# Optimization experiments

Measured on AMD Instinct MI355X. Metric: run time of the kernel, lower is better.

## Reference

```python
import jax, jax.numpy as jnp
import numpy as np
from jax import lax

EPS = 1e-31
V, L, B, T = 30000, 400, 16, 145
E, EH, DH, ENC, COMB = 100, 150, 200, 300, 500
SOS = 1


def setup_inputs() -> dict:
    key = jax.random.key(0)
    ks = jax.random.split(key, 32)
    def p(i, shape):
        return jax.random.normal(ks[i], shape, dtype=jnp.float32) * 0.05
    return {
        "input_tensor": jax.random.randint(ks[0], (L, B), 0, V),
        "embedding": p(1, (V, E)),
        "enc_Wih_f": p(2, (3 * EH, E)), "enc_Whh_f": p(3, (3 * EH, EH)),
        "enc_bih_f": p(4, (3 * EH,)), "enc_bhh_f": p(5, (3 * EH,)),
        "enc_Wih_b": p(6, (3 * EH, E)), "enc_Whh_b": p(7, (3 * EH, EH)),
        "enc_bih_b": p(8, (3 * EH,)), "enc_bhh_b": p(9, (3 * EH,)),
        "adapter_W": p(10, (DH, ENC)), "adapter_b": p(11, (DH,)),
        "dec_Wih": p(12, (3 * DH, E)), "dec_Whh": p(13, (3 * DH, DH)),
        "dec_bih": p(14, (3 * DH,)), "dec_bhh": p(15, (3 * DH,)),
        "bil_W": p(16, (1, DH, ENC)), "bil_b": p(17, (1,)),
        "cover_weight": jax.random.uniform(ks[18], (1,), dtype=jnp.float32),
        "ptr_W": p(19, (1, COMB)), "ptr_b": p(20, (1,)),
        "preout_W": p(21, (E, COMB)), "preout_b": p(22, (E,)),
        "out_b": p(23, (V,)),
    }


def _gru_cell(x, h, Wih, Whh, bih, bhh):
    # torch GRU cell semantics (gates ordered r, z, n)
    gi = x @ Wih.T + bih
    gh = h @ Whh.T + bhh
    ir, iz, i_n = jnp.split(gi, 3, axis=-1)
    hr, hz, hn = jnp.split(gh, 3, axis=-1)
    r = jax.nn.sigmoid(ir + hr)
    z = jax.nn.sigmoid(iz + hz)
    n = jnp.tanh(i_n + r * hn)
    return (1.0 - z) * n + z * h


def _run_gru(emb, Wih, Whh, bih, bhh):
    # emb: [L, B, E] -> outputs [L, B, H], final hidden [B, H]
    h0 = jnp.zeros((emb.shape[1], Whh.shape[1]), emb.dtype)
    def step(h, x):
        h = _gru_cell(x, h, Wih, Whh, bih, bhh)
        return h, h
    hT, ys = lax.scan(step, h0, emb)
    return ys, hT


def reference(input_tensor, embedding,
              enc_Wih_f, enc_Whh_f, enc_bih_f, enc_bhh_f,
              enc_Wih_b, enc_Whh_b, enc_bih_b, enc_bhh_b,
              adapter_W, adapter_b,
              dec_Wih, dec_Whh, dec_bih, dec_bhh,
              bil_W, bil_b, cover_weight,
              ptr_W, ptr_b, preout_W, preout_b, out_b):
    # ----- encoder: bidirectional single-layer GRU -----
    emb = embedding[input_tensor]                       # [L, B, E]
    out_f, h_f = _run_gru(emb, enc_Wih_f, enc_Whh_f, enc_bih_f, enc_bhh_f)
    out_r, h_b = _run_gru(emb[::-1], enc_Wih_b, enc_Whh_b, enc_bih_b, enc_bhh_b)
    enc_out = jnp.concatenate([out_f, out_r[::-1]], axis=-1)   # [L, B, 300]
    enc_hidden = jnp.concatenate([h_f, h_b], axis=-1)          # [B, 300]
    h0 = enc_hidden @ adapter_W.T + adapter_b                  # enc_dec_adapter -> [B, 200]

    enc_word_idx = input_tensor.T                              # [B, L]
    batch_idx = jnp.arange(enc_out.shape[1])[:, None]

    # ----- decoder: greedy loop with enc attention + coverage + pointer-gen -----
    def dec_step(carry, _):
        h, cover, tok = carry
        x = embedding[tok]                                     # [B, E]
        h = _gru_cell(x, h, dec_Wih, dec_Whh, dec_bih, dec_bhh)
        # bilinear energy: h W e + b, plus coverage term
        hW = h @ bil_W[0]                                      # [B, 300]
        energy = jnp.einsum('be,lbe->lb', hW, enc_out) + bil_b[0]
        energy = energy + cover_weight[0] * jnp.log(cover.T + EPS)
        attn = jax.nn.softmax(energy, axis=0)                  # [L, B], softmax over enc steps
        context = jnp.einsum('lbe,lb->be', enc_out, attn)      # [B, 300]
        combined = jnp.concatenate([h, context], axis=-1)      # [B, 500]
        pre = combined @ preout_W.T + preout_b                 # [B, 100]
        logits = pre @ embedding.T + out_b                     # tied output embedding [B, V]
        p_ptr = jax.nn.sigmoid(combined @ ptr_W.T + ptr_b)     # [B, 1]
        gen = jax.nn.softmax(logits, axis=1)
        attn_bl = attn.T                                       # [B, L]
        out = (1.0 - p_ptr) * gen
        out = out.at[batch_idx, enc_word_idx].add(p_ptr * attn_bl)
        new_tok = jnp.argmax(out, axis=1)
        return (h, cover + attn_bl, new_tok), out

    cover0 = jnp.zeros(enc_word_idx.shape, emb.dtype)
    tok0 = jnp.full((enc_out.shape[1],), SOS, dtype=input_tensor.dtype)
    _, outputs = lax.scan(dec_step, (h0, cover0, tok0), None, length=T)
    return outputs  # [T, B, V] pointer-generator mixture probabilities
```

## Files before the change

kernel.cpp:

```cpp
#include <hip/hip_runtime.h>

namespace {

constexpr int Vv=30000, Ll=400, Bb=16, Tt=145;
constexpr int Ee=100, EHh=150, DHh=200, ENc=300;
constexpr int SOS_TOK=1;
constexpr int NB=256, NT=512;

constexpr long SO_EMB = 0;
constexpr long SO_GIF = SO_EMB + 6400L*100;
constexpr long SO_GIB = SO_GIF + 6400L*450;
constexpr long SO_ENC = SO_GIB + 6400L*450;
constexpr long SO_WCAT= SO_GIF;

constexpr int RH    = 0;
constexpr int REXP  = 3200;
constexpr int RCTX  = 9600;
constexpr int RPREH = 22912;
constexpr int RPSUM = 24576;
constexpr int RPMAX = 28672;
constexpr int RCAND = 36864;
constexpr int RING_SZ = 49664;

constexpr long OFF_M    = 0;
constexpr long OFF_N    = OFF_M + 6400L*200;
constexpr long OFF_Q    = OFF_N + 6400L*100;
constexpr long OFF_HENC = OFF_Q + 6400;
constexpr long OFF_H0   = OFF_HENC + 4800;
constexpr long OFF_COVER= OFF_H0 + 3200;
constexpr long OFF_R143 = OFF_COVER + 8192;
constexpr long OFF_R144 = OFF_R143 + RING_SZ;
constexpr long WS_F32_END = OFF_R144 + RING_SZ;
constexpr long IWS_BYTE  = ((WS_F32_END*4 + 255)/256)*256;
constexpr int ISVL=0, IGV=6400, IGLS=12800, ICG0=19216, INGR=23328;
constexpr long BAR_BYTE  = ((IWS_BYTE + 23344L*4 + 255)/256)*256;
constexpr int FH  =0;
constexpr int FS1 =256;
constexpr int FCTX=320;
constexpr int FS4 =448;
constexpr int ABRT=704;

struct Args {
  const int* itok;
  const float* emb;
  const float* Wfih; const float* Wfhh; const float* bfih; const float* bfhh;
  const float* Wbih; const float* Wbhh; const float* bbih; const float* bbhh;
  const float* adW; const float* adb;
  const float* dWih; const float* dWhh; const float* dbih; const float* dbhh;
  const float* bilW; const float* bilb; const float* cw;
  const float* ptrW; const float* ptrb;
  const float* preW; const float* preb; const float* outb;
  float* out; float* ws; int* iws; int* bar;
};

__device__ __forceinline__ int chunkStart(int c){ return c*117 + (c<48? c:48); }
__device__ __forceinline__ int chunkSize(int c){ return 117 + (c<48?1:0); }
__device__ __forceinline__ float sigm(float x){ return 1.f/(1.f+expf(-x)); }
__device__ __forceinline__ unsigned long long packvi(float val, int v){
  return ((unsigned long long)__float_as_uint(val)<<32) | (unsigned)(~(unsigned)v);
}
__device__ __forceinline__ void ast(float* p, float v){
  __hip_atomic_store(p, v, __ATOMIC_RELAXED, __HIP_MEMORY_SCOPE_AGENT); }
__device__ __forceinline__ void astu(unsigned long long* p, unsigned long long v){
  __hip_atomic_store(p, v, __ATOMIC_RELAXED, __HIP_MEMORY_SCOPE_AGENT); }
__device__ __forceinline__ int aldi(const int* p){
  return __hip_atomic_load(p, __ATOMIC_RELAXED, __HIP_MEMORY_SCOPE_AGENT); }
__device__ __forceinline__ void asti(int* p, int v){
  __hip_atomic_store(p, v, __ATOMIC_RELAXED, __HIP_MEMORY_SCOPE_AGENT); }

__device__ __forceinline__ float* ringBase(const Args& a, int t){
  if (t<=142) return a.out + (long)(t+2)*480000;
  return a.ws + (t==143 ? OFF_R143 : OFF_R144);
}

__device__ __forceinline__ void setFlag(int* f, int v){
  asm volatile("s_waitcnt vmcnt(0) lgkmcnt(0)" ::: "memory");
  __syncthreads();
  if (threadIdx.x==0) asti(f, v);
}
__device__ __forceinline__ void waitFlags(const int* flags, int n, int target, int* abrt){
  if (threadIdx.x<64){
    int lane=threadIdx.x;
    long it=0;
    for (;;){
      int mn=0x7FFFFFFF;
      for (int i=lane;i<n;i+=64){
        int v=aldi(flags+i);
        if (v<mn) mn=v;
      }
      if (__all(mn>=target)) break;
      __builtin_amdgcn_s_sleep(2);
      if (++it > 400000L){ asti(abrt,1); break; }
      if ((it&255)==0 && aldi(abrt)!=0) break;
    }
  }
  __syncthreads();
}

__device__ __forceinline__ void hbarF(int* bar, int epoch){
  asm volatile("s_waitcnt vmcnt(0) lgkmcnt(0)" ::: "memory");
  __syncthreads();
  if (threadIdx.x==0){
    __builtin_amdgcn_fence(__ATOMIC_RELEASE, "agent");
    asti(bar+FH+blockIdx.x, epoch);
  }
  waitFlags(bar+FH, NB, epoch, bar+ABRT);
  if (threadIdx.x==0)
    __builtin_amdgcn_fence(__ATOMIC_ACQUIRE, "agent");
  __syncthreads();
}

__device__ void sortB(const Args& a, int b, char* smem){
  int tid=threadIdx.x;
  int* key=(int*)smem;
  key[tid] = (tid<Ll)? (a.itok[tid*16+b]*Ll + tid) : 0x7FFFFFFF;
  __syncthreads();
  for (int k=2;k<=512;k<<=1){
    for (int j=k>>1;j>0;j>>=1){
      int ixj = tid^j;
      if (ixj>tid){
        int x=key[tid], y=key[ixj];
        bool up = ((tid&k)==0);
        if ((x>y)==up){ key[tid]=y; key[ixj]=x; }
      }
      __syncthreads();
    }
  }
  int* ngS=(int*)(smem+2048);
  if (tid==0){
    int* svl=a.iws+ISVL+b*400; int* gvv=a.iws+IGV+b*400;
    int* gls=a.iws+IGLS+b*401;
    int ng=0, prev=-1;
    for (int i=0;i<400;i++){
      int kk=key[i]; int tok=kk/400, l=kk-tok*400;
      svl[i]=l;
      if (tok!=prev){ gvv[ng]=tok; gls[ng]=i; ng++; prev=tok; }
    }
    gls[ng]=400;
    a.iws[INGR+b]=ng;
    ngS[0]=ng;
  }
  __syncthreads();
  int ng=ngS[0];
  const int* gvv=a.iws+IGV+b*400;
  for (int c=tid;c<=256;c+=NT){
    int target=(c<256)? chunkStart(c) : 0x7FFFFFFF;
    int lo=0,hi=ng;
    while(lo<hi){ int mid=(lo+hi)>>1; if (gvv[mid]<target) lo=mid+1; else hi=mid; }
    a.iws[ICG0+b*257+c]=lo;
  }
}

template<int MODE>
__device__ void tileGemm(const Args& a, char* smem){
  float* Xl=(float*)smem;
  float* Wl=(float*)(smem+25600);
  const int K   = MODE? 300 : 100;
  const int NC  = MODE? 301 : 900;
  const int nCT = MODE? 5 : 15;
  const int nTiles = 100*nCT;
  const float* X = a.out + (MODE? SO_ENC : SO_EMB);
  int ty=threadIdx.x>>4, tx=threadIdx.x&15;
  for (int tile=blockIdx.x; tile<nTiles; tile+=NB){
    int rt=tile%100, ct=tile/100;
    int r0=rt*64, c0=ct*64;
    float acc[2][4];
    #pragma unroll
    for (int i=0;i<2;i++){
      #pragma unroll
      for (int j=0;j<4;j++) acc[i][j]=0.f;
    }
    for (int k0=0;k0<K;k0+=100){
      for (int i=threadIdx.x;i<1600;i+=NT){
        int rr=i/25, e4=i%25;
        ((float4*)Xl)[rr*25+e4] = *((const float4*)(X + (long)(r0+rr)*K + k0) + e4);
      }
      for (int i=threadIdx.x;i<1600;i+=NT){
        int rr=i/25, e4=i%25; int c=c0+rr;
        float4 w={0.f,0.f,0.f,0.f};
        if (c<NC){
          const float* wr;
          if (MODE==0) wr = (c<450)? (a.Wfih + (long)c*100) : (a.Wbih + (long)(c-450)*100);
          else         wr = a.out + SO_WCAT + (long)c*300 + k0;
          w = *((const float4*)wr + e4);
        }
        ((float4*)Wl)[rr*25+e4]=w;
      }
      __syncthreads();
      for (int k4=0;k4<25;k4++){
        float4 a4[2], b4[4];
        #pragma unroll
        for (int i=0;i<2;i++) a4[i]=((float4*)Xl)[(ty*2+i)*25+k4];
        #pragma unroll
        for (int j=0;j<4;j++) b4[j]=((float4*)Wl)[(tx*4+j)*25+k4];
        #pragma unroll
        for (int i=0;i<2;i++){
          #pragma unroll
          for (int j=0;j<4;j++){
            acc[i][j] += a4[i].x*b4[j].x;
            acc[i][j] += a4[i].y*b4[j].y;
            acc[i][j] += a4[i].z*b4[j].z;
            acc[i][j] += a4[i].w*b4[j].w;
          }
        }
      }
      __syncthreads();
    }
    #pragma unroll
    for (int i=0;i<2;i++){
      #pragma unroll
      for (int j=0;j<4;j++){
        int r=r0+ty*2+i, c=c0+tx*4+j;
        if (c<NC){
          if (MODE==0){
            int dir=c/450, cc=c-dir*450;
            float v=acc[i][j] + (dir? a.bbih : a.bfih)[cc];
            a.out[(dir?SO_GIB:SO_GIF) + (long)r*450 + cc]=v;
          } else {
            if (c<200)      a.ws[OFF_M + (long)r*200 + c]=acc[i][j];
            else if (c<300) a.ws[OFF_N + (long)r*100 + (c-200)]=acc[i][j];
            else            a.ws[OFF_Q + r]=acc[i][j];
          }
        }
      }
    }
  }
}

__device__ void encoderPhase(const Args& a, int bid, char* smem){
  int tid=threadIdx.x;
  int dir=bid>>4, b=bid&15;
  float* hbuf=(float*)smem;
  float* gbuf=(float*)(smem+2048);
  float* pacc=(float*)(smem+8192);
  const float* Whh = dir? a.Wbhh : a.Wfhh;
  const float* bhh = dir? a.bbhh : a.bfhh;
  const float* giBase = a.out + (dir? SO_GIB : SO_GIF);
  int ks=tid/150; int j=tid-ks*150;
  bool act = (ks<3);
  float w[3][50];
  if (act){
    #pragma unroll
    for (int g=0;g<3;g++)
      for (int k=0;k<50;k++)
        w[g][k]=Whh[(long)(g*150+j)*150 + ks*50 + k];
  }
  float b0=0,b1=0,b2=0;
  if (act && ks==0){ b0=bhh[j]; b1=bhh[150+j]; b2=bhh[300+j]; }
  for (int i=tid;i<192;i+=NT) hbuf[i]=0.f;
  {
    int l0 = dir? 399 : 0;
    for (int i=tid;i<450;i+=NT) gbuf[i]=giBase[((long)l0*16+b)*450+i];
  }
  __syncthreads();
  for (int s=0;s<400;s++){
    int p=s&1;
    int l=dir? 399-s : s;
    if (tid>=450 && s+1<400){
      int ln=dir? 399-(s+1) : s+1;
      for (int i=tid-450;i<450;i+=62) gbuf[(p^1)*452+i]=giBase[((long)ln*16+b)*450+i];
    }
    if (act){
      float ar=0.f, az=0.f, an=0.f;
      const float* hr=hbuf + p*192 + ks*64;
      #pragma unroll
      for (int k4=0;k4<12;k4++){
        float4 h4=*(const float4*)(hr + k4*4);
        ar+=h4.x*w[0][k4*4+0]; ar+=h4.y*w[0][k4*4+1]; ar+=h4.z*w[0][k4*4+2]; ar+=h4.w*w[0][k4*4+3];
        az+=h4.x*w[1][k4*4+0]; az+=h4.y*w[1][k4*4+1]; az+=h4.z*w[1][k4*4+2]; az+=h4.w*w[1][k4*4+3];
        an+=h4.x*w[2][k4*4+0]; an+=h4.y*w[2][k4*4+1]; an+=h4.z*w[2][k4*4+2]; an+=h4.w*w[2][k4*4+3];
      }
      {
        float h48=hr[48], h49=hr[49];
        ar+=h48*w[0][48]+h49*w[0][49];
        az+=h48*w[1][48]+h49*w[1][49];
        an+=h48*w[2][48]+h49*w[2][49];
      }
      pacc[(ks*3+0)*152+j]=ar;
      pacc[(ks*3+1)*152+j]=az;
      pacc[(ks*3+2)*152+j]=an;
    }
    __syncthreads();
    if (act && ks==0){
      float ar=pacc[(0*3+0)*152+j]+pacc[(1*3+0)*152+j]+pacc[(2*3+0)*152+j];
      float az=pacc[(0*3+1)*152+j]+pacc[(1*3+1)*152+j]+pacc[(2*3+1)*152+j];
      float an=pacc[(0*3+2)*152+j]+pacc[(1*3+2)*152+j]+pacc[(2*3+2)*152+j];
      const float* gi=gbuf + p*452;
      float r=sigm(gi[j]      + ar + b0);
      float z=sigm(gi[150+j]  + az + b1);
      float n=tanhf(gi[300+j] + r*(an + b2));
      int slot=(j/50)*64 + (j%50);
      float hold=hbuf[p*192+slot];
      float hv=(1.f-z)*n + z*hold;
      hbuf[(p^1)*192+slot]=hv;
      a.out[SO_ENC + ((long)l*16+b)*300 + dir*150 + j]=hv;
      if (s==399) a.ws[OFF_HENC + ((long)dir*16+b)*150 + j]=hv;
    }
    __syncthreads();
  }
}

__device__ void s1Phase(const Args& a, int bid, int t, float* slot, const float* slotP, char* smem){
  int tid=threadIdx.x;
  float* xw=(float*)smem;
  float* hw=(float*)(smem+6400);
  int* tokL=(int*)(smem+19200);
  if (t==0){
    if (tid<16) tokL[tid]=SOS_TOK;
  } else {
    const float* psum = slotP + RPSUM;
    const unsigned long long* pmax=(const unsigned long long*)(slotP + RPMAX);
    int b=tid>>5, ln=tid&31;
    float zs=0.f;
    for (int c=ln;c<256;c+=32) zs += psum[b*256+c];
    #pragma unroll
    for (int off=16;off;off>>=1) zs+=__shfl_xor(zs,off,32);
    float Z=zs;
    unsigned long long best=0;
    for (int c=ln;c<256;c+=32){
      unsigned long long pm=pmax[b*256+c];
      float ev=__uint_as_float((unsigned)(pm>>32));
      int v=(int)(~(unsigned)(pm & 0xFFFFFFFFull));
      unsigned long long pk=packvi(ev/Z, v);
      if (pk>best) best=pk;
    }
    int ng=a.iws[INGR+b];
    const float* cd=slotP + RCAND + b*800;
    const int* gvv=a.iws+IGV+b*400;
    for (int g=ln;g<ng;g+=32){
      unsigned long long pk=packvi(cd[g*2]/Z + cd[g*2+1], gvv[g]);
      if (pk>best) best=pk;
    }
    #pragma unroll
    for (int off=16;off;off>>=1){
      unsigned long long o=__shfl_xor(best,off,32);
      if (o>best) best=o;
    }
    if (ln==0) tokL[b]=(int)(~(unsigned)(best & 0xFFFFFFFFull));
  }
  __syncthreads();
  for (int i=tid;i<1600;i+=NT){ int b=i/100, e=i-b*100; xw[i]=a.emb[(long)tokL[b]*100+e]; }
  const float* hprev = (t==0)? (a.ws+OFF_H0) : (slotP+RH);
  for (int i=tid;i<3200;i+=NT) hw[i]=hprev[i];
  __syncthreads();
  {
    int pair=tid>>3, lane=tid&7;
    int uj=pair>>4, b=pair&15;
    int j=bid*4+uj;
    float air=0,aiz=0,ain=0,ahr=0,ahz=0,ahn=0;
    const float* x=xw+b*100;
    for (int k=lane;k<100;k+=8){
      float xv=x[k];
      air+=xv*a.dWih[(long)j*100+k];
      aiz+=xv*a.dWih[(long)(200+j)*100+k];
      ain+=xv*a.dWih[(long)(400+j)*100+k];
    }
    const float* h=hw+b*200;
    for (int k=lane;k<200;k+=8){
      float hv=h[k];
      ahr+=hv*a.dWhh[(long)j*200+k];
      ahz+=hv*a.dWhh[(long)(200+j)*200+k];
      ahn+=hv*a.dWhh[(long)(400+j)*200+k];
    }
    #pragma unroll
    for (int off=4;off;off>>=1){
      air+=__shfl_xor(air,off,8); aiz+=__shfl_xor(aiz,off,8); ain+=__shfl_xor(ain,off,8);
      ahr+=__shfl_xor(ahr,off,8); ahz+=__shfl_xor(ahz,off,8); ahn+=__shfl_xor(ahn,off,8);
    }
    if (lane==0){
      float r=sigm(air + a.dbih[j]     + ahr + a.dbhh[j]);
      float z=sigm(aiz + a.dbih[200+j] + ahz + a.dbhh[200+j]);
      float n=tanhf(ain + a.dbih[400+j] + r*(ahn + a.dbhh[400+j]));
      ast(slot + RH + b*200 + j, (1.f-z)*n + z*h[j]);
    }
  }
  {
    int nrows=(bid==49)?3:2;
    int unit=tid>>3, lane=tid&7;
    int jsub=unit>>4, b=unit&15;
    if (jsub<nrows){
      int j=bid*2+jsub;
      const float* w=(j<100)? (a.preW + (long)j*500) : a.ptrW;
      const float* h=hw+b*200;
      float acc=0.f;
      for (int k=lane;k<200;k+=8) acc+=h[k]*w[k];
      #pragma unroll
      for (int off=4;off;off>>=1) acc+=__shfl_xor(acc,off,8);
      if (lane==0) ast(slot + RPREH + b*104 + j, acc);
    }
  }
}

__device__ void s2ePhase(const Args& a, int idx, int t, float* slot, const float* slotP, char* smem){
  int tid=threadIdx.x;
  int b=idx&15, lg=idx>>4, l0=lg*50;
  float* hb =(float*)smem;
  float* exl=(float*)(smem+1024);
  float* zaS=(float*)(smem+1280);
  const float* hsrc=slot + RH + b*200;
  for (int i=tid;i<200;i+=NT) hb[i]=hsrc[i];
  if (tid==0){
    float za=0.f;
    if (t>0){
      float s0=0,s1=0,s2=0,s3=0;
      s0=slotP[RCTX+(b*8+0)*104+101]+slotP[RCTX+(b*8+1)*104+101];
      s1=slotP[RCTX+(b*8+2)*104+101]+slotP[RCTX+(b*8+3)*104+101];
      s2=slotP[RCTX+(b*8+4)*104+101]+slotP[RCTX+(b*8+5)*104+101];
      s3=slotP[RCTX+(b*8+6)*104+101]+slotP[RCTX+(b*8+7)*104+101];
      za=(s0+s1)+(s2+s3);
    }
    zaS[0]=za;
  }
  __syncthreads();
  int unit=tid>>3, lane=tid&7;
  if (unit<50){
    int l=l0+unit;
    const float* Mr=a.ws+OFF_M + (long)(l*16+b)*200;
    float acc=0.f;
    for (int k=lane;k<200;k+=8) acc+=hb[k]*Mr[k];
    #pragma unroll
    for (int off=4;off;off>>=1) acc+=__shfl_xor(acc,off,8);
    if (lane==0){
      float* cov=a.ws+OFF_COVER + (b*8+lg)*64 + unit;
      float cv=*cov;
      if (t>0) cv += slotP[REXP + b*400 + l] / zaS[0];
      *cov=cv;
      float en = acc + a.bilb[0] + a.cw[0]*logf(cv + 1e-31f);
      float ex = expf(en);
      ast(slot + REXP + b*400 + l, ex);
      exl[unit]=ex;
    }
  }
  __syncthreads();
  int u2=tid>>2, lane2=tid&3;
  if (u2<102){
    int k=u2; float acc=0.f;
    if (k<100){
      for (int ll=lane2;ll<50;ll+=4) acc+=exl[ll]*a.ws[OFF_N + (long)((l0+ll)*16+b)*100 + k];
    } else if (k==100){
      for (int ll=lane2;ll<50;ll+=4) acc+=exl[ll]*a.ws[OFF_Q + (l0+ll)*16 + b];
    } else {
      for (int ll=lane2;ll<50;ll+=4) acc+=exl[ll];
    }
    #pragma unroll
    for (int off=2;off;off>>=1) acc+=__shfl_xor(acc,off,4);
    if (lane2==0) ast(slot + RCTX + (b*8+lg)*104 + k, acc);
  }
}

__device__ void wbPhase(const Args& a, int c, int tr, const float* slotP, float* exPrev, char* smem){
  int tid=threadIdx.x;
  int v0=chunkStart(c), nv=chunkSize(c);
  float* zpart=(float*)(smem+8192);
  float* zl1=(float*)(smem+10240);
  float* pp1=(float*)(smem+10304);
  const float* psum = slotP + RPSUM;
  {
    int b=tid&15, seg=tid>>4;
    float z=0.f;
    for (int cc=seg;cc<256;cc+=32) z+=psum[b*256+cc];
    zpart[seg*16+b]=z;
  }
  __syncthreads();
  if (tid<16){
    int b=tid;
    float z=0.f;
    for (int s2=0;s2<32;s2++) z+=zpart[s2*16+b];
    zl1[b]=z;
    float za0=slotP[RCTX+(b*8+0)*104+101]+slotP[RCTX+(b*8+1)*104+101];
    float za1=slotP[RCTX+(b*8+2)*104+101]+slotP[RCTX+(b*8+3)*104+101];
    float za2=slotP[RCTX+(b*8+4)*104+101]+slotP[RCTX+(b*8+5)*104+101];
    float za3=slotP[RCTX+(b*8+6)*104+101]+slotP[RCTX+(b*8+7)*104+101];
    float qa0=slotP[RCTX+(b*8+0)*104+100]+slotP[RCTX+(b*8+1)*104+100];
    float qa1=slotP[RCTX+(b*8+2)*104+100]+slotP[RCTX+(b*8+3)*104+100];
    float qa2=slotP[RCTX+(b*8+4)*104+100]+slotP[RCTX+(b*8+5)*104+100];
    float qa3=slotP[RCTX+(b*8+6)*104+100]+slotP[RCTX+(b*8+7)*104+100];
    float za=(za0+za1)+(za2+za3);
    float qc=(qa0+qa1)+(qa2+qa3);
    pp1[b]=sigm(qc/za + slotP[RPREH + b*104 + 100] + a.ptrb[0]);
  }
  __syncthreads();
  if (tid<16){
    int b=tid;
    const int* cg0=a.iws+ICG0+b*257; const int* gvv=a.iws+IGV+b*400;
    const float* cd=slotP + RCAND + b*800;
    for (int g=cg0[c];g<cg0[c+1];g++){
      exPrev[(gvv[g]-v0)*17+b] += cd[g*2+1]*zl1[b];
    }
  }
  __syncthreads();
  {
    int tot=nv*16;
    for (int u=tid;u<tot;u+=NT){
      int b2=u/nv, vl=u-b2*nv;
      float sc=(1.f-pp1[b2])/zl1[b2];
      __builtin_nontemporal_store(exPrev[vl*17+b2]*sc,
                                  &a.out[((long)tr*16+b2)*30000 + v0+vl]);
    }
  }
  __syncthreads();
}

__device__ void s4Phase(const Args& a, int c, int t, float* slot, float* exCur, char* smem){
  int tid=threadIdx.x;
  int v0=chunkStart(c), nv=chunkSize(c);
  float* preL=(float*)smem;
  float* zaL =(float*)(smem+6400);
  float* ppqL=(float*)(smem+6464);
  if (tid<16){
    int b=tid;
    float za0=slot[RCTX+(b*8+0)*104+101]+slot[RCTX+(b*8+1)*104+101];
    float za1=slot[RCTX+(b*8+2)*104+101]+slot[RCTX+(b*8+3)*104+101];
    float za2=slot[RCTX+(b*8+4)*104+101]+slot[RCTX+(b*8+5)*104+101];
    float za3=slot[RCTX+(b*8+6)*104+101]+slot[RCTX+(b*8+7)*104+101];
    float qa0=slot[RCTX+(b*8+0)*104+100]+slot[RCTX+(b*8+1)*104+100];
    float qa1=slot[RCTX+(b*8+2)*104+100]+slot[RCTX+(b*8+3)*104+100];
    float qa2=slot[RCTX+(b*8+4)*104+100]+slot[RCTX+(b*8+5)*104+100];
    float qa3=slot[RCTX+(b*8+6)*104+100]+slot[RCTX+(b*8+7)*104+100];
    float za=(za0+za1)+(za2+za3);
    float qc=(qa0+qa1)+(qa2+qa3);
    zaL[b]=za;
    ppqL[b]=sigm(qc/za + slot[RPREH + b*104 + 100] + a.ptrb[0]);
  }
  __syncthreads();
  for (int u=tid;u<1600;u+=NT){
    int b=u/100, k=u-b*100;
    float s0=slot[RCTX+(b*8+0)*104+k]+slot[RCTX+(b*8+1)*104+k];
    float s1=slot[RCTX+(b*8+2)*104+k]+slot[RCTX+(b*8+3)*104+k];
    float s2=slot[RCTX+(b*8+4)*104+k]+slot[RCTX+(b*8+5)*104+k];
    float s3=slot[RCTX+(b*8+6)*104+k]+slot[RCTX+(b*8+7)*104+k];
    float sv=(s0+s1)+(s2+s3);
    preL[u]=sv/zaL[b] + slot[RPREH + b*104 + k] + a.preb[k];
  }
  __syncthreads();
  int bloc=tid&15;
  float4 preg[25];
  {
    const float4* p4=(const float4*)(preL + bloc*100);
    #pragma unroll
    for (int e4=0;e4<25;e4++) preg[e4]=p4[e4];
  }
  int nu=nv*16;
  const float4* emb4=(const float4*)a.emb;
  for (int u=tid;u<nu;u+=NT){
    int vl=u>>4; int v=v0+vl;
    float acc=a.outb[v];
    const float4* er=emb4 + (long)v*25;
    #pragma unroll
    for (int e4=0;e4<25;e4++){
      float4 A=er[e4], Bv=preg[e4];
      acc += A.x*Bv.x + A.y*Bv.y + A.z*Bv.z + A.w*Bv.w;
    }
    exCur[vl*17+bloc]=expf(acc);
  }
  __syncthreads();
  {
    int b=tid>>5, sg=tid&31;
    float s=0.f; unsigned long long m=0;
    for (int vl=sg;vl<nv;vl+=32){
      float ex=exCur[vl*17+b];
      s+=ex;
      unsigned long long pk=packvi(ex, v0+vl);
      if (pk>m) m=pk;
    }
    #pragma unroll
    for (int off=16;off;off>>=1){
      s+=__shfl_xor(s,off,32);
      unsigned long long om=__shfl_xor(m,off,32);
      if (om>m) m=om;
    }
    if (sg==0){
      ast(slot + RPSUM + b*256 + c, s);
      astu((unsigned long long*)(slot + RPMAX) + b*256 + c, m);
    }
  }
  if (tid<16){
    int b=tid;
    const int* cg0=a.iws+ICG0+b*257; const int* gvv=a.iws+IGV+b*400;
    const int* gls=a.iws+IGLS+b*401; const int* svl=a.iws+ISVL+b*400;
    float* cd=slot + RCAND + b*800;
    float pfac=ppqL[b]/(1.f-ppqL[b]);
    for (int g=cg0[c];g<cg0[c+1];g++){
      int v=gvv[g];
      float gs=0.f;
      for (int i2=gls[g];i2<gls[g+1];i2++) gs+=slot[REXP + b*400 + svl[i2]];
      ast(cd+g*2,   exCur[(v-v0)*17+b]);
      ast(cd+g*2+1, pfac*gs/zaL[b]);
    }
  }
}

__global__ void kInitBar(int* bar){
  int t=threadIdx.x;
  if (t<1024) bar[t]=0;
}

__global__ __launch_bounds__(NT,1) void mega(Args a){
  __shared__ __align__(16) char smem[53248];
  int bid=blockIdx.x, tid=threadIdx.x;
  int* bar=a.bar;
  int* abrt=bar+ABRT;
  float* exBuf0=(float*)(smem+36864);
  float* exBuf1=(float*)(smem+44928);

  if (bid<16){
    sortB(a,bid,smem);
  } else {
    for (long i=(long)(bid-16)*NT+tid; i<640000; i+=240L*NT){
      long pair=i/100; int e=(int)(i-pair*100);
      a.out[SO_EMB+i]=a.emb[(long)a.itok[pair]*100+e];
    }
    for (int i=(bid-16)*NT+tid; i<8192; i+=240*NT) a.ws[OFF_COVER+i]=0.f;
  }
  hbarF(bar,1);

  tileGemm<0>(a,smem);
  hbarF(bar,2);

  if (bid<32) encoderPhase(a,bid,smem);
  hbarF(bar,3);

  for (long i=(long)bid*NT+tid; i<90300; i+=(long)NB*NT){
    int rr=(int)(i/300), k=(int)(i-(long)rr*300);
    float v;
    if (rr<200)      v=a.bilW[(long)rr*300+k];
    else if (rr<300) v=a.preW[(long)(rr-200)*500+200+k];
    else             v=a.ptrW[200+k];
    a.out[SO_WCAT+i]=v;
  }
  if (bid>=32 && bid<48){
    int b=bid-32;
    int unit=tid>>1, lane=tid&1;
    if (unit<200){
      int j=unit;
      const float* w=a.adW+(long)j*300 + lane*150;
      const float* hh=a.ws+OFF_HENC + ((long)lane*16+b)*150;
      float acc=0.f;
      for (int e=0;e<150;e++) acc+=hh[e]*w[e];
      acc+=__shfl_xor(acc,1,2);
      if (lane==0) a.ws[OFF_H0 + b*200 + j]=acc + a.adb[j];
    }
  }
  hbarF(bar,4);

  tileGemm<1>(a,smem);
  hbarF(bar,5);

  for (int t=0;t<Tt;t++){
    int q=t&1;
    float* exCur  = q? exBuf1 : exBuf0;
    float* exPrev = q? exBuf0 : exBuf1;
    float* slot   = ringBase(a,t);
    float* slotP  = (t>0)? ringBase(a,t-1) : (float*)0;
    if (bid<50){
      if (t>0) waitFlags(bar+FS4, 256, t, abrt);
      s1Phase(a,bid,t,slot,slotP,smem);
      setFlag(bar+FS1+bid, t+1);
      if (t>0) wbPhase(a,bid,t-1,slotP,exPrev,smem);
    } else if (bid>=64 && bid<192){
      waitFlags(bar+FS1, 50, t+1, abrt);
      s2ePhase(a,bid-64,t,slot,slotP,smem);
      setFlag(bar+FCTX+(bid-64), t+1);
      if (t>0) wbPhase(a,bid,t-1,slotP,exPrev,smem);
    } else {
      if (t>0){
        waitFlags(bar+FS4, 256, t, abrt);
        wbPhase(a,bid,t-1,slotP,exPrev,smem);
      }
    }
    waitFlags(bar+FCTX, 128, t+1, abrt);
    s4Phase(a,bid,t,slot,exCur,smem);
    setFlag(bar+FS4+bid, t+1);
  }
  waitFlags(bar+FS4, 256, Tt, abrt);
  wbPhase(a,bid,Tt-1,ringBase(a,Tt-1),exBuf0,smem);
}

}

extern "C" void kernel_launch(void* const* d_in, const int* in_sizes, int n_in,
                              void* d_out, int out_size, void* d_ws, size_t ws_size,
                              hipStream_t stream) {
  Args a;
  a.itok=(const int*)d_in[0];
  a.emb =(const float*)d_in[1];
  a.Wfih=(const float*)d_in[2]; a.Wfhh=(const float*)d_in[3];
  a.bfih=(const float*)d_in[4]; a.bfhh=(const float*)d_in[5];
  a.Wbih=(const float*)d_in[6]; a.Wbhh=(const float*)d_in[7];
  a.bbih=(const float*)d_in[8]; a.bbhh=(const float*)d_in[9];
  a.adW =(const float*)d_in[10]; a.adb=(const float*)d_in[11];
  a.dWih=(const float*)d_in[12]; a.dWhh=(const float*)d_in[13];
  a.dbih=(const float*)d_in[14]; a.dbhh=(const float*)d_in[15];
  a.bilW=(const float*)d_in[16]; a.bilb=(const float*)d_in[17];
  a.cw  =(const float*)d_in[18];
  a.ptrW=(const float*)d_in[19]; a.ptrb=(const float*)d_in[20];
  a.preW=(const float*)d_in[21]; a.preb=(const float*)d_in[22];
  a.outb=(const float*)d_in[23];
  a.out =(float*)d_out;
  a.ws  =(float*)d_ws;
  a.iws =(int*)((char*)d_ws + IWS_BYTE);
  a.bar =(int*)((char*)d_ws + BAR_BYTE);

  kInitBar<<<dim3(1),dim3(1024),0,stream>>>(a.bar);
  void* kargs[] = { (void*)&a };
  hipLaunchCooperativeKernel(reinterpret_cast<const void*>(mega),
                             dim3(NB), dim3(NT), kargs, 0, stream);
}
```

Baseline: 11.34 ms.

## Move decoder exchange buffers to double-buffered workspace and split pre-out projection into separate blocks

Per-step exchange data (hidden state, attention exps, context partials, pre-out, partial sums, pmax, candidates) moves from a ring of slots inside the output tensor to dedicated double-buffered workspace arrays with batch-innermost layouts for psum/pmax/exp. The pre-out/pointer projection, formerly done by the 50 GRU blocks, now runs in 16 separate blocks in parallel with the attention blocks, shortening the GRU stage on the critical path. Spin-wait sleeps are lengthened with a short-sleep warmup. The risks are extra flags to wait on (144 instead of 128) and atomic loads on all exchange reads.

```diff
diff --git a/kernel.cpp b/kernel.cpp
--- a/kernel.cpp
+++ b/kernel.cpp
@@ -2,8 +2,7 @@
 
 namespace {
 
-constexpr int Vv=30000, Ll=400, Bb=16, Tt=145;
-constexpr int Ee=100, EHh=150, DHh=200, ENc=300;
+constexpr int Vv=30000, Ll=400, Tt=145;
 constexpr int SOS_TOK=1;
 constexpr int NB=256, NT=512;
 
@@ -13,32 +12,28 @@
 constexpr long SO_ENC = SO_GIB + 6400L*450;
 constexpr long SO_WCAT= SO_GIF;
 
-constexpr int RH    = 0;
-constexpr int REXP  = 3200;
-constexpr int RCTX  = 9600;
-constexpr int RPREH = 22912;
-constexpr int RPSUM = 24576;
-constexpr int RPMAX = 28672;
-constexpr int RCAND = 36864;
-constexpr int RING_SZ = 49664;
-
 constexpr long OFF_M    = 0;
 constexpr long OFF_N    = OFF_M + 6400L*200;
 constexpr long OFF_Q    = OFF_N + 6400L*100;
 constexpr long OFF_HENC = OFF_Q + 6400;
-constexpr long OFF_H0   = OFF_HENC + 4800;
-constexpr long OFF_COVER= OFF_H0 + 3200;
-constexpr long OFF_R143 = OFF_COVER + 8192;
-constexpr long OFF_R144 = OFF_R143 + RING_SZ;
-constexpr long WS_F32_END = OFF_R144 + RING_SZ;
-constexpr long IWS_BYTE  = ((WS_F32_END*4 + 255)/256)*256;
+constexpr long OFF_HDEC = OFF_HENC + 4800;
+constexpr long OFF_COVER= OFF_HDEC + 6400;
+constexpr long OFF_EXPE = OFF_COVER + 8192;
+constexpr long OFF_PREH = OFF_EXPE + 12800;
+constexpr long OFF_CTXP = OFF_PREH + 3328;
+constexpr long OFF_PSUM = OFF_CTXP + 26624;
+constexpr long OFF_CAND = OFF_PSUM + 8192;
+constexpr long WS_F32_END = OFF_CAND + 25600;
+constexpr long PMAX_BYTE = ((WS_F32_END*4 + 255)/256)*256;
+constexpr long IWS_BYTE  = PMAX_BYTE + 2L*4096*8;
 constexpr int ISVL=0, IGV=6400, IGLS=12800, ICG0=19216, INGR=23328;
 constexpr long BAR_BYTE  = ((IWS_BYTE + 23344L*4 + 255)/256)*256;
 constexpr int FH  =0;
 constexpr int FS1 =256;
 constexpr int FCTX=320;
-constexpr int FS4 =448;
-constexpr int ABRT=704;
+constexpr int FS4 =480;
+constexpr int ABRT=736;
+constexpr int BARN=768;
 
 struct Args {
   const int* itok;
@@ -50,7 +45,7 @@
   const float* bilW; const float* bilb; const float* cw;
   const float* ptrW; const float* ptrb;
   const float* preW; const float* preb; const float* outb;
-  float* out; float* ws; int* iws; int* bar;
+  float* out; float* ws; unsigned long long* pmax; int* iws; int* bar;
 };
 
 __device__ __forceinline__ int chunkStart(int c){ return c*117 + (c<48? c:48); }
@@ -59,19 +54,18 @@
 __device__ __forceinline__ unsigned long long packvi(float val, int v){
   return ((unsigned long long)__float_as_uint(val)<<32) | (unsigned)(~(unsigned)v);
 }
+__device__ __forceinline__ float ald(const float* p){
+  return __hip_atomic_load(p, __ATOMIC_RELAXED, __HIP_MEMORY_SCOPE_AGENT); }
 __device__ __forceinline__ void ast(float* p, float v){
   __hip_atomic_store(p, v, __ATOMIC_RELAXED, __HIP_MEMORY_SCOPE_AGENT); }
+__device__ __forceinline__ unsigned long long aldu(const unsigned long long* p){
+  return __hip_atomic_load(p, __ATOMIC_RELAXED, __HIP_MEMORY_SCOPE_AGENT); }
 __device__ __forceinline__ void astu(unsigned long long* p, unsigned long long v){
   __hip_atomic_store(p, v, __ATOMIC_RELAXED, __HIP_MEMORY_SCOPE_AGENT); }
 __device__ __forceinline__ int aldi(const int* p){
   return __hip_atomic_load(p, __ATOMIC_RELAXED, __HIP_MEMORY_SCOPE_AGENT); }
 __device__ __forceinline__ void asti(int* p, int v){
   __hip_atomic_store(p, v, __ATOMIC_RELAXED, __HIP_MEMORY_SCOPE_AGENT); }
-
-__device__ __forceinline__ float* ringBase(const Args& a, int t){
-  if (t<=142) return a.out + (long)(t+2)*480000;
-  return a.ws + (t==143 ? OFF_R143 : OFF_R144);
-}
 
 __device__ __forceinline__ void setFlag(int* f, int v){
   asm volatile("s_waitcnt vmcnt(0) lgkmcnt(0)" ::: "memory");
@@ -89,20 +83,21 @@
         if (v<mn) mn=v;
       }
       if (__all(mn>=target)) break;
-      __builtin_amdgcn_s_sleep(2);
-      if (++it > 400000L){ asti(abrt,1); break; }
-      if ((it&255)==0 && aldi(abrt)!=0) break;
-    }
-  }
-  __syncthreads();
-}
-
-__device__ __forceinline__ void hbarF(int* bar, int epoch){
+      if (it<4) __builtin_amdgcn_s_sleep(8);
+      else      __builtin_amdgcn_s_sleep(96);
+      if (++it > 250000L){ asti(abrt,1); break; }
+      if ((it&127)==0 && aldi(abrt)!=0) break;
+    }
+  }
+  __syncthreads();
+}
+__device__ __forceinline__ void hbarF(const Args& a, int epoch){
+  int* bar=a.bar;
   asm volatile("s_waitcnt vmcnt(0) lgkmcnt(0)" ::: "memory");
   __syncthreads();
   if (threadIdx.x==0){
     __builtin_amdgcn_fence(__ATOMIC_RELEASE, "agent");
-    asti(bar+FH+blockIdx.x, epoch);
+    asti(bar+FH+(int)blockIdx.x, epoch);
   }
   waitFlags(bar+FH, NB, epoch, bar+ABRT);
   if (threadIdx.x==0)
@@ -300,35 +295,35 @@
   }
 }
 
-__device__ void s1Phase(const Args& a, int bid, int t, float* slot, const float* slotP, char* smem){
+__device__ void s1Phase(const Args& a, int bid, int t, char* smem){
   int tid=threadIdx.x;
+  int q=t&1, p1=q^1;
   float* xw=(float*)smem;
   float* hw=(float*)(smem+6400);
   int* tokL=(int*)(smem+19200);
   if (t==0){
     if (tid<16) tokL[tid]=SOS_TOK;
   } else {
-    const float* psum = slotP + RPSUM;
-    const unsigned long long* pmax=(const unsigned long long*)(slotP + RPMAX);
     int b=tid>>5, ln=tid&31;
     float zs=0.f;
-    for (int c=ln;c<256;c+=32) zs += psum[b*256+c];
+    for (int c=ln;c<256;c+=32) zs+=ald(&a.ws[OFF_PSUM + ((long)p1*256+c)*16 + b]);
     #pragma unroll
     for (int off=16;off;off>>=1) zs+=__shfl_xor(zs,off,32);
     float Z=zs;
     unsigned long long best=0;
     for (int c=ln;c<256;c+=32){
-      unsigned long long pm=pmax[b*256+c];
+      unsigned long long pm=aldu(&a.pmax[((long)p1*256+c)*16+b]);
       float ev=__uint_as_float((unsigned)(pm>>32));
       int v=(int)(~(unsigned)(pm & 0xFFFFFFFFull));
       unsigned long long pk=packvi(ev/Z, v);
       if (pk>best) best=pk;
     }
     int ng=a.iws[INGR+b];
-    const float* cd=slotP + RCAND + b*800;
+    const float* cd=a.ws+OFF_CAND + ((long)p1*16+b)*800;
     const int* gvv=a.iws+IGV+b*400;
     for (int g=ln;g<ng;g+=32){
-      unsigned long long pk=packvi(cd[g*2]/Z + cd[g*2+1], gvv[g]);
+      float v1=ald(&cd[g*2]), v2=ald(&cd[g*2+1]);
+      unsigned long long pk=packvi(v1/Z + v2, gvv[g]);
       if (pk>best) best=pk;
     }
     #pragma unroll
@@ -340,73 +335,58 @@
   }
   __syncthreads();
   for (int i=tid;i<1600;i+=NT){ int b=i/100, e=i-b*100; xw[i]=a.emb[(long)tokL[b]*100+e]; }
-  const float* hprev = (t==0)? (a.ws+OFF_H0) : (slotP+RH);
-  for (int i=tid;i<3200;i+=NT) hw[i]=hprev[i];
-  __syncthreads();
-  {
-    int pair=tid>>3, lane=tid&7;
-    int uj=pair>>4, b=pair&15;
-    int j=bid*4+uj;
-    float air=0,aiz=0,ain=0,ahr=0,ahz=0,ahn=0;
-    const float* x=xw+b*100;
-    for (int k=lane;k<100;k+=8){
-      float xv=x[k];
-      air+=xv*a.dWih[(long)j*100+k];
-      aiz+=xv*a.dWih[(long)(200+j)*100+k];
-      ain+=xv*a.dWih[(long)(400+j)*100+k];
-    }
-    const float* h=hw+b*200;
-    for (int k=lane;k<200;k+=8){
-      float hv=h[k];
-      ahr+=hv*a.dWhh[(long)j*200+k];
-      ahz+=hv*a.dWhh[(long)(200+j)*200+k];
-      ahn+=hv*a.dWhh[(long)(400+j)*200+k];
-    }
-    #pragma unroll
-    for (int off=4;off;off>>=1){
-      air+=__shfl_xor(air,off,8); aiz+=__shfl_xor(aiz,off,8); ain+=__shfl_xor(ain,off,8);
-      ahr+=__shfl_xor(ahr,off,8); ahz+=__shfl_xor(ahz,off,8); ahn+=__shfl_xor(ahn,off,8);
-    }
-    if (lane==0){
-      float r=sigm(air + a.dbih[j]     + ahr + a.dbhh[j]);
-      float z=sigm(aiz + a.dbih[200+j] + ahz + a.dbhh[200+j]);
-      float n=tanhf(ain + a.dbih[400+j] + r*(ahn + a.dbhh[400+j]));
-      ast(slot + RH + b*200 + j, (1.f-z)*n + z*h[j]);
-    }
-  }
-  {
-    int nrows=(bid==49)?3:2;
-    int unit=tid>>3, lane=tid&7;
-    int jsub=unit>>4, b=unit&15;
-    if (jsub<nrows){
-      int j=bid*2+jsub;
-      const float* w=(j<100)? (a.preW + (long)j*500) : a.ptrW;
-      const float* h=hw+b*200;
-      float acc=0.f;
-      for (int k=lane;k<200;k+=8) acc+=h[k]*w[k];
-      #pragma unroll
-      for (int off=4;off;off>>=1) acc+=__shfl_xor(acc,off,8);
-      if (lane==0) ast(slot + RPREH + b*104 + j, acc);
-    }
-  }
-}
-
-__device__ void s2ePhase(const Args& a, int idx, int t, float* slot, const float* slotP, char* smem){
+  for (int i=tid;i<3200;i+=NT) hw[i]=ald(&a.ws[OFF_HDEC + (long)p1*3200 + i]);
+  __syncthreads();
+  int pair=tid>>3, lane=tid&7;
+  int uj=pair>>4, b=pair&15;
+  int j=bid*4+uj;
+  float air=0,aiz=0,ain=0,ahr=0,ahz=0,ahn=0;
+  const float* x=xw+b*100;
+  for (int k=lane;k<100;k+=8){
+    float xv=x[k];
+    air+=xv*a.dWih[(long)j*100+k];
+    aiz+=xv*a.dWih[(long)(200+j)*100+k];
+    ain+=xv*a.dWih[(long)(400+j)*100+k];
+  }
+  const float* h=hw+b*200;
+  for (int k=lane;k<200;k+=8){
+    float hv=h[k];
+    ahr+=hv*a.dWhh[(long)j*200+k];
+    ahz+=hv*a.dWhh[(long)(200+j)*200+k];
+    ahn+=hv*a.dWhh[(long)(400+j)*200+k];
+  }
+  #pragma unroll
+  for (int off=4;off;off>>=1){
+    air+=__shfl_xor(air,off,8); aiz+=__shfl_xor(aiz,off,8); ain+=__shfl_xor(ain,off,8);
+    ahr+=__shfl_xor(ahr,off,8); ahz+=__shfl_xor(ahz,off,8); ahn+=__shfl_xor(ahn,off,8);
+  }
+  if (lane==0){
+    float r=sigm(air + a.dbih[j]     + ahr + a.dbhh[j]);
+    float z=sigm(aiz + a.dbih[200+j] + ahz + a.dbhh[200+j]);
+    float n=tanhf(ain + a.dbih[400+j] + r*(ahn + a.dbhh[400+j]));
+    ast(&a.ws[OFF_HDEC + (long)q*3200 + b*200 + j], (1.f-z)*n + z*h[j]);
+  }
+}
+
+__device__ void s2ePhase(const Args& a, int idx, int t, char* smem){
   int tid=threadIdx.x;
+  int q=t&1, p1=q^1;
   int b=idx&15, lg=idx>>4, l0=lg*50;
   float* hb =(float*)smem;
   float* exl=(float*)(smem+1024);
   float* zaS=(float*)(smem+1280);
-  const float* hsrc=slot + RH + b*200;
-  for (int i=tid;i<200;i+=NT) hb[i]=hsrc[i];
+  for (int i=tid;i<200;i+=NT) hb[i]=ald(&a.ws[OFF_HDEC + (long)q*3200 + b*200 + i]);
   if (tid==0){
     float za=0.f;
     if (t>0){
-      float s0=0,s1=0,s2=0,s3=0;
-      s0=slotP[RCTX+(b*8+0)*104+101]+slotP[RCTX+(b*8+1)*104+101];
-      s1=slotP[RCTX+(b*8+2)*104+101]+slotP[RCTX+(b*8+3)*104+101];
-      s2=slotP[RCTX+(b*8+4)*104+101]+slotP[RCTX+(b*8+5)*104+101];
-      s3=slotP[RCTX+(b*8+6)*104+101]+slotP[RCTX+(b*8+7)*104+101];
+      float s0=ald(&a.ws[OFF_CTXP+(((long)p1*16+b)*8+0)*104+101])
+             +ald(&a.ws[OFF_CTXP+(((long)p1*16+b)*8+1)*104+101]);
+      float s1=ald(&a.ws[OFF_CTXP+(((long)p1*16+b)*8+2)*104+101])
+             +ald(&a.ws[OFF_CTXP+(((long)p1*16+b)*8+3)*104+101]);
+      float s2=ald(&a.ws[OFF_CTXP+(((long)p1*16+b)*8+4)*104+101])
+             +ald(&a.ws[OFF_CTXP+(((long)p1*16+b)*8+5)*104+101]);
+      float s3=ald(&a.ws[OFF_CTXP+(((long)p1*16+b)*8+6)*104+101])
+             +ald(&a.ws[OFF_CTXP+(((long)p1*16+b)*8+7)*104+101]);
       za=(s0+s1)+(s2+s3);
     }
     zaS[0]=za;
@@ -423,11 +403,11 @@
     if (lane==0){
       float* cov=a.ws+OFF_COVER + (b*8+lg)*64 + unit;
       float cv=*cov;
-      if (t>0) cv += slotP[REXP + b*400 + l] / zaS[0];
+      if (t>0) cv += ald(&a.ws[OFF_EXPE + (long)p1*6400 + l*16 + b]) / zaS[0];
       *cov=cv;
       float en = acc + a.bilb[0] + a.cw[0]*logf(cv + 1e-31f);
       float ex = expf(en);
-      ast(slot + REXP + b*400 + l, ex);
+      ast(&a.ws[OFF_EXPE + (long)q*6400 + l*16 + b], ex);
       exl[unit]=ex;
     }
   }
@@ -444,93 +424,60 @@
     }
     #pragma unroll
     for (int off=2;off;off>>=1) acc+=__shfl_xor(acc,off,4);
-    if (lane2==0) ast(slot + RCTX + (b*8+lg)*104 + k, acc);
-  }
-}
-
-__device__ void wbPhase(const Args& a, int c, int tr, const float* slotP, float* exPrev, char* smem){
+    if (lane2==0) ast(&a.ws[OFF_CTXP + (((long)q*16+b)*8+lg)*104 + k], acc);
+  }
+}
+
+__device__ void phPhase(const Args& a, int b, int t, char* smem){
   int tid=threadIdx.x;
-  int v0=chunkStart(c), nv=chunkSize(c);
-  float* zpart=(float*)(smem+8192);
-  float* zl1=(float*)(smem+10240);
-  float* pp1=(float*)(smem+10304);
-  const float* psum = slotP + RPSUM;
-  {
-    int b=tid&15, seg=tid>>4;
-    float z=0.f;
-    for (int cc=seg;cc<256;cc+=32) z+=psum[b*256+cc];
-    zpart[seg*16+b]=z;
-  }
-  __syncthreads();
-  if (tid<16){
-    int b=tid;
-    float z=0.f;
-    for (int s2=0;s2<32;s2++) z+=zpart[s2*16+b];
-    zl1[b]=z;
-    float za0=slotP[RCTX+(b*8+0)*104+101]+slotP[RCTX+(b*8+1)*104+101];
-    float za1=slotP[RCTX+(b*8+2)*104+101]+slotP[RCTX+(b*8+3)*104+101];
-    float za2=slotP[RCTX+(b*8+4)*104+101]+slotP[RCTX+(b*8+5)*104+101];
-    float za3=slotP[RCTX+(b*8+6)*104+101]+slotP[RCTX+(b*8+7)*104+101];
-    float qa0=slotP[RCTX+(b*8+0)*104+100]+slotP[RCTX+(b*8+1)*104+100];
-    float qa1=slotP[RCTX+(b*8+2)*104+100]+slotP[RCTX+(b*8+3)*104+100];
-    float qa2=slotP[RCTX+(b*8+4)*104+100]+slotP[RCTX+(b*8+5)*104+100];
-    float qa3=slotP[RCTX+(b*8+6)*104+100]+slotP[RCTX+(b*8+7)*104+100];
-    float za=(za0+za1)+(za2+za3);
-    float qc=(qa0+qa1)+(qa2+qa3);
-    pp1[b]=sigm(qc/za + slotP[RPREH + b*104 + 100] + a.ptrb[0]);
-  }
-  __syncthreads();
-  if (tid<16){
-    int b=tid;
-    const int* cg0=a.iws+ICG0+b*257; const int* gvv=a.iws+IGV+b*400;
-    const float* cd=slotP + RCAND + b*800;
-    for (int g=cg0[c];g<cg0[c+1];g++){
-      exPrev[(gvv[g]-v0)*17+b] += cd[g*2+1]*zl1[b];
-    }
-  }
-  __syncthreads();
-  {
-    int tot=nv*16;
-    for (int u=tid;u<tot;u+=NT){
-      int b2=u/nv, vl=u-b2*nv;
-      float sc=(1.f-pp1[b2])/zl1[b2];
-      __builtin_nontemporal_store(exPrev[vl*17+b2]*sc,
-                                  &a.out[((long)tr*16+b2)*30000 + v0+vl]);
-    }
-  }
-  __syncthreads();
-}
-
-__device__ void s4Phase(const Args& a, int c, int t, float* slot, float* exCur, char* smem){
+  int q=t&1;
+  float* hb=(float*)smem;
+  for (int i=tid;i<200;i+=NT) hb[i]=ald(&a.ws[OFF_HDEC + (long)q*3200 + b*200 + i]);
+  __syncthreads();
+  int unit=tid>>2, lane=tid&3;
+  if (unit<101){
+    const float* w=(unit<100)? (a.preW + (long)unit*500) : a.ptrW;
+    float acc=0.f;
+    for (int k=lane;k<200;k+=4) acc+=hb[k]*w[k];
+    #pragma unroll
+    for (int off=2;off;off>>=1) acc+=__shfl_xor(acc,off,4);
+    if (lane==0) ast(&a.ws[OFF_PREH + ((long)q*16+b)*104 + unit], acc);
+  }
+}
+
+__device__ void s4Phase(const Args& a, int c, int t, float* exCur, char* smem){
   int tid=threadIdx.x;
+  int q=t&1;
   int v0=chunkStart(c), nv=chunkSize(c);
   float* preL=(float*)smem;
   float* zaL =(float*)(smem+6400);
   float* ppqL=(float*)(smem+6464);
   if (tid<16){
     int b=tid;
-    float za0=slot[RCTX+(b*8+0)*104+101]+slot[RCTX+(b*8+1)*104+101];
-    float za1=slot[RCTX+(b*8+2)*104+101]+slot[RCTX+(b*8+3)*104+101];
-    float za2=slot[RCTX+(b*8+4)*104+101]+slot[RCTX+(b*8+5)*104+101];
-    float za3=slot[RCTX+(b*8+6)*104+101]+slot[RCTX+(b*8+7)*104+101];
-    float qa0=slot[RCTX+(b*8+0)*104+100]+slot[RCTX+(b*8+1)*104+100];
-    float qa1=slot[RCTX+(b*8+2)*104+100]+slot[RCTX+(b*8+3)*104+100];
-    float qa2=slot[RCTX+(b*8+4)*104+100]+slot[RCTX+(b*8+5)*104+100];
-    float qa3=slot[RCTX+(b*8+6)*104+100]+slot[RCTX+(b*8+7)*104+100];
+    long base=((long)q*16+b)*8;
+    float za0=ald(&a.ws[OFF_CTXP+(base+0)*104+101])+ald(&a.ws[OFF_CTXP+(base+1)*104+101]);
+    float za1=ald(&a.ws[OFF_CTXP+(base+2)*104+101])+ald(&a.ws[OFF_CTXP+(base+3)*104+101]);
+    float za2=ald(&a.ws[OFF_CTXP+(base+4)*104+101])+ald(&a.ws[OFF_CTXP+(base+5)*104+101]);
+    float za3=ald(&a.ws[OFF_CTXP+(base+6)*104+101])+ald(&a.ws[OFF_CTXP+(base+7)*104+101]);
+    float qa0=ald(&a.ws[OFF_CTXP+(base+0)*104+100])+ald(&a.ws[OFF_CTXP+(base+1)*104+100]);
+    float qa1=ald(&a.ws[OFF_CTXP+(base+2)*104+100])+ald(&a.ws[OFF_CTXP+(base+3)*104+100]);
+    float qa2=ald(&a.ws[OFF_CTXP+(base+4)*104+100])+ald(&a.ws[OFF_CTXP+(base+5)*104+100]);
+    float qa3=ald(&a.ws[OFF_CTXP+(base+6)*104+100])+ald(&a.ws[OFF_CTXP+(base+7)*104+100]);
     float za=(za0+za1)+(za2+za3);
     float qc=(qa0+qa1)+(qa2+qa3);
     zaL[b]=za;
-    ppqL[b]=sigm(qc/za + slot[RPREH + b*104 + 100] + a.ptrb[0]);
+    ppqL[b]=sigm(qc/za + ald(&a.ws[OFF_PREH + ((long)q*16+b)*104 + 100]) + a.ptrb[0]);
   }
   __syncthreads();
   for (int u=tid;u<1600;u+=NT){
     int b=u/100, k=u-b*100;
-    float s0=slot[RCTX+(b*8+0)*104+k]+slot[RCTX+(b*8+1)*104+k];
-    float s1=slot[RCTX+(b*8+2)*104+k]+slot[RCTX+(b*8+3)*104+k];
-    float s2=slot[RCTX+(b*8+4)*104+k]+slot[RCTX+(b*8+5)*104+k];
-    float s3=slot[RCTX+(b*8+6)*104+k]+slot[RCTX+(b*8+7)*104+k];
+    long base=((long)q*16+b)*8;
+    float s0=ald(&a.ws[OFF_CTXP+(base+0)*104+k])+ald(&a.ws[OFF_CTXP+(base+1)*104+k]);
+    float s1=ald(&a.ws[OFF_CTXP+(base+2)*104+k])+ald(&a.ws[OFF_CTXP+(base+3)*104+k]);
+    float s2=ald(&a.ws[OFF_CTXP+(base+4)*104+k])+ald(&a.ws[OFF_CTXP+(base+5)*104+k]);
+    float s3=ald(&a.ws[OFF_CTXP+(base+6)*104+k])+ald(&a.ws[OFF_CTXP+(base+7)*104+k]);
     float sv=(s0+s1)+(s2+s3);
-    preL[u]=sv/zaL[b] + slot[RPREH + b*104 + k] + a.preb[k];
+    preL[u]=sv/zaL[b] + ald(&a.ws[OFF_PREH + ((long)q*16+b)*104 + k]) + a.preb[k];
   }
   __syncthreads();
   int bloc=tid&15;
@@ -570,29 +517,81 @@
       if (om>m) m=om;
     }
     if (sg==0){
-      ast(slot + RPSUM + b*256 + c, s);
-      astu((unsigned long long*)(slot + RPMAX) + b*256 + c, m);
+      ast(&a.ws[OFF_PSUM + ((long)q*256+c)*16 + b], s);
+      astu(&a.pmax[((long)q*256+c)*16 + b], m);
     }
   }
   if (tid<16){
     int b=tid;
     const int* cg0=a.iws+ICG0+b*257; const int* gvv=a.iws+IGV+b*400;
     const int* gls=a.iws+IGLS+b*401; const int* svl=a.iws+ISVL+b*400;
-    float* cd=slot + RCAND + b*800;
+    float* cd=a.ws+OFF_CAND + ((long)q*16+b)*800;
     float pfac=ppqL[b]/(1.f-ppqL[b]);
     for (int g=cg0[c];g<cg0[c+1];g++){
       int v=gvv[g];
       float gs=0.f;
-      for (int i2=gls[g];i2<gls[g+1];i2++) gs+=slot[REXP + b*400 + svl[i2]];
+      for (int i2=gls[g];i2<gls[g+1];i2++) gs+=ald(&a.ws[OFF_EXPE + (long)q*6400 + svl[i2]*16 + b]);
       ast(cd+g*2,   exCur[(v-v0)*17+b]);
       ast(cd+g*2+1, pfac*gs/zaL[b]);
     }
   }
 }
 
+__device__ void wbPhase(const Args& a, int c, int p1, int tr, float* exPrev, char* smem){
+  int tid=threadIdx.x;
+  int v0=chunkStart(c), nv=chunkSize(c);
+  float* zpart=(float*)(smem+8192);
+  float* zl1=(float*)(smem+10240);
+  float* pp1=(float*)(smem+10304);
+  {
+    int b=tid&15, seg=tid>>4;
+    float z=0.f;
+    for (int cc=seg;cc<256;cc+=32) z+=ald(&a.ws[OFF_PSUM + ((long)p1*256+cc)*16 + b]);
+    zpart[seg*16+b]=z;
+  }
+  __syncthreads();
+  if (tid<16){
+    int b=tid;
+    float z=0.f;
+    for (int s2=0;s2<32;s2++) z+=zpart[s2*16+b];
+    zl1[b]=z;
+    long base=((long)p1*16+b)*8;
+    float za0=ald(&a.ws[OFF_CTXP+(base+0)*104+101])+ald(&a.ws[OFF_CTXP+(base+1)*104+101]);
+    float za1=ald(&a.ws[OFF_CTXP+(base+2)*104+101])+ald(&a.ws[OFF_CTXP+(base+3)*104+101]);
+    float za2=ald(&a.ws[OFF_CTXP+(base+4)*104+101])+ald(&a.ws[OFF_CTXP+(base+5)*104+101]);
+    float za3=ald(&a.ws[OFF_CTXP+(base+6)*104+101])+ald(&a.ws[OFF_CTXP+(base+7)*104+101]);
+    float qa0=ald(&a.ws[OFF_CTXP+(base+0)*104+100])+ald(&a.ws[OFF_CTXP+(base+1)*104+100]);
+    float qa1=ald(&a.ws[OFF_CTXP+(base+2)*104+100])+ald(&a.ws[OFF_CTXP+(base+3)*104+100]);
+    float qa2=ald(&a.ws[OFF_CTXP+(base+4)*104+100])+ald(&a.ws[OFF_CTXP+(base+5)*104+100]);
+    float qa3=ald(&a.ws[OFF_CTXP+(base+6)*104+100])+ald(&a.ws[OFF_CTXP+(base+7)*104+100]);
+    float za=(za0+za1)+(za2+za3);
+    float qc=(qa0+qa1)+(qa2+qa3);
+    pp1[b]=sigm(qc/za + ald(&a.ws[OFF_PREH + ((long)p1*16+b)*104 + 100]) + a.ptrb[0]);
+  }
+  __syncthreads();
+  if (tid<16){
+    int b=tid;
+    const int* cg0=a.iws+ICG0+b*257; const int* gvv=a.iws+IGV+b*400;
+    const float* cd=a.ws+OFF_CAND + ((long)p1*16+b)*800;
+    for (int g=cg0[c];g<cg0[c+1];g++){
+      exPrev[(gvv[g]-v0)*17+b] += ald(&cd[g*2+1])*zl1[b];
+    }
+  }
+  __syncthreads();
+  {
+    int tot=nv*16;
+    for (int u=tid;u<tot;u+=NT){
+      int b2=u/nv, vl=u-b2*nv;
+      float sc=(1.f-pp1[b2])/zl1[b2];
+      __builtin_nontemporal_store(exPrev[vl*17+b2]*sc,
+                                  &a.out[((long)tr*16+b2)*30000 + v0+vl]);
+    }
+  }
+  __syncthreads();
+}
+
 __global__ void kInitBar(int* bar){
-  int t=threadIdx.x;
-  if (t<1024) bar[t]=0;
+  for (int i=threadIdx.x;i<BARN;i+=1024) bar[i]=0;
 }
 
 __global__ __launch_bounds__(NT,1) void mega(Args a){
@@ -612,14 +611,11 @@
     }
     for (int i=(bid-16)*NT+tid; i<8192; i+=240*NT) a.ws[OFF_COVER+i]=0.f;
   }
-  hbarF(bar,1);
-
+  hbarF(a,1);
   tileGemm<0>(a,smem);
-  hbarF(bar,2);
-
+  hbarF(a,2);
   if (bid<32) encoderPhase(a,bid,smem);
-  hbarF(bar,3);
-
+  hbarF(a,3);
   for (long i=(long)bid*NT+tid; i<90300; i+=(long)NB*NT){
     int rr=(int)(i/300), k=(int)(i-(long)rr*300);
     float v;
@@ -638,42 +634,45 @@
       float acc=0.f;
       for (int e=0;e<150;e++) acc+=hh[e]*w[e];
       acc+=__shfl_xor(acc,1,2);
-      if (lane==0) a.ws[OFF_H0 + b*200 + j]=acc + a.adb[j];
-    }
-  }
-  hbarF(bar,4);
-
+      if (lane==0) a.ws[OFF_HDEC + 1L*3200 + b*200 + j]=acc + a.adb[j];
+    }
+  }
+  hbarF(a,4);
   tileGemm<1>(a,smem);
-  hbarF(bar,5);
+  hbarF(a,5);
 
   for (int t=0;t<Tt;t++){
     int q=t&1;
     float* exCur  = q? exBuf1 : exBuf0;
     float* exPrev = q? exBuf0 : exBuf1;
-    float* slot   = ringBase(a,t);
-    float* slotP  = (t>0)? ringBase(a,t-1) : (float*)0;
+    int p1=q^1;
     if (bid<50){
       if (t>0) waitFlags(bar+FS4, 256, t, abrt);
-      s1Phase(a,bid,t,slot,slotP,smem);
+      s1Phase(a,bid,t,smem);
       setFlag(bar+FS1+bid, t+1);
-      if (t>0) wbPhase(a,bid,t-1,slotP,exPrev,smem);
+      if (t>0) wbPhase(a,bid,p1,t-1,exPrev,smem);
     } else if (bid>=64 && bid<192){
       waitFlags(bar+FS1, 50, t+1, abrt);
-      s2ePhase(a,bid-64,t,slot,slotP,smem);
+      s2ePhase(a,bid-64,t,smem);
       setFlag(bar+FCTX+(bid-64), t+1);
-      if (t>0) wbPhase(a,bid,t-1,slotP,exPrev,smem);
+      if (t>0) wbPhase(a,bid,p1,t-1,exPrev,smem);
+    } else if (bid>=192 && bid<208){
+      waitFlags(bar+FS1, 50, t+1, abrt);
+      phPhase(a,bid-192,t,smem);
+      setFlag(bar+FCTX+128+(bid-192), t+1);
+      if (t>0) wbPhase(a,bid,p1,t-1,exPrev,smem);
     } else {
       if (t>0){
         waitFlags(bar+FS4, 256, t, abrt);
-        wbPhase(a,bid,t-1,slotP,exPrev,smem);
-      }
-    }
-    waitFlags(bar+FCTX, 128, t+1, abrt);
-    s4Phase(a,bid,t,slot,exCur,smem);
+        wbPhase(a,bid,p1,t-1,exPrev,smem);
+      }
+    }
+    waitFlags(bar+FCTX, 144, t+1, abrt);
+    s4Phase(a,bid,t,exCur,smem);
     setFlag(bar+FS4+bid, t+1);
   }
   waitFlags(bar+FS4, 256, Tt, abrt);
-  wbPhase(a,bid,Tt-1,ringBase(a,Tt-1),exBuf0,smem);
+  wbPhase(a,bid,(Tt-1)&1,Tt-1,((Tt-1)&1)?exBuf1:exBuf0,smem);
 }
 
 }
@@ -698,11 +697,13 @@
   a.outb=(const float*)d_in[23];
   a.out =(float*)d_out;
   a.ws  =(float*)d_ws;
+  a.pmax=(unsigned long long*)((char*)d_ws + PMAX_BYTE);
   a.iws =(int*)((char*)d_ws + IWS_BYTE);
   a.bar =(int*)((char*)d_ws + BAR_BYTE);
 
+  hipError_t e0 = hipSuccess; (void)e0;
   kInitBar<<<dim3(1),dim3(1024),0,stream>>>(a.bar);
   void* kargs[] = { (void*)&a };
-  hipLaunchCooperativeKernel(reinterpret_cast<const void*>(mega),
-                             dim3(NB), dim3(NT), kargs, 0, stream);
-}
+  e0 = hipLaunchCooperativeKernel(reinterpret_cast<const void*>(mega),
+                                  dim3(NB), dim3(NT), kargs, 0, stream);
+}
```

After: 11.57 ms. 2.0% more time.
